# Optimization experiments

Measured on AMD Instinct MI355X. Metric: run time of the kernel, lower is better.

## Reference

```python
import jax, jax.numpy as jnp
import numpy as np

B, T, D, H = 2, 2048, 1024, 16
HD = D // H  # 64


def setup_inputs() -> dict:
    key = jax.random.key(0)
    ks = jax.random.split(key, 9)
    w = lambda k, shp: (jax.random.normal(k, shp, jnp.float32) * 0.02)
    return {
        "x": jax.random.normal(ks[0], (B, T, D), jnp.float32),
        "Wq": w(ks[1], (D, D)), "bq": jnp.zeros((D,), jnp.float32),
        "Wk": w(ks[2], (D, D)), "bk": jnp.zeros((D,), jnp.float32),
        "Wv": w(ks[3], (D, D)), "bv": jnp.zeros((D,), jnp.float32),
        "Wo": w(ks[4], (D, D)), "bo": jnp.zeros((D,), jnp.float32),
        "Wqs": w(ks[5], (3, HD)), "bqs": jnp.zeros((3,), jnp.float32),
        "Wks": w(ks[6], (3, HD)), "bks": jnp.zeros((3,), jnp.float32),
        "Wvs": w(ks[7], (3, HD)), "bvs": jnp.zeros((3,), jnp.float32),
        "temp": jnp.float32(1.0),
    }


def reference(x, Wq, bq, Wk, bk, Wv, bv, Wo, bo, Wqs, bqs, Wks, bks, Wvs, bvs, temp):
    Bx, Tx, Dx = x.shape
    # project and split heads: [B,H,T,HD]
    split = lambda y: y.reshape(Bx, Tx, H, HD).transpose(0, 2, 1, 3)
    q = split(x @ Wq.T + bq)
    k = split(x @ Wk.T + bk)
    v = split(x @ Wv.T + bv)
    # STP projections to 3-d: [B,H,T,3]
    q_stp = q @ Wqs.T + bqs
    k3 = k @ Wks.T + bks
    v3 = v @ Wvs.T + bvs
    # cross-product term (note: original's layernormed k_sub/v_sub are dead code)
    cross_kv = jnp.cross(k3, v3, axis=-1)  # [B,H,T,3]
    scores = (jnp.einsum('bhqd,bhkd->bhqk', q, k)
              + jnp.einsum('bhqc,bhkc->bhqk', q_stp, cross_kv)) * temp
    attn = jax.nn.softmax(scores, axis=-1)
    out = jnp.einsum('bhqk,bhkd->bhqd', attn, v)  # [B,H,T,HD]
    out = out.transpose(0, 2, 1, 3).reshape(Bx, Tx, Dx)
    return out @ Wo.T + bo
```

## Files before the change

### kernel.cpp

```cpp
#include <hip/hip_runtime.h>
#include <stdint.h>

typedef unsigned short u16;
typedef unsigned int u32;
typedef __attribute__((ext_vector_type(8))) short bf16x8;
typedef __attribute__((ext_vector_type(4))) float f32x4;
typedef __attribute__((ext_vector_type(4))) unsigned int u32x4;

__device__ __forceinline__ u16 f2b(float f) {
    union { float f; u32 u; } t; t.f = f;
    return (u16)((t.u + 0x7FFFu + ((t.u >> 16) & 1u)) >> 16);
}
__device__ __forceinline__ u32 pack2(float a, float b) {
    return (u32)f2b(a) | ((u32)f2b(b) << 16);
}
__device__ __forceinline__ u32 cvtpk2(float lo, float hi) {
    u32 r;
    asm("v_cvt_pk_bf16_f32 %0, %1, %2" : "=v"(r) : "v"(lo), "v"(hi));
    return r;
}
__device__ __forceinline__ void permlane32_swap(u32& a, u32& b) {
    asm("v_permlane32_swap_b32 %0, %1" : "+v"(a), "+v"(b));
}
__device__ __forceinline__ void permlane16_swap(u32& a, u32& b) {
    asm("v_permlane16_swap_b32 %0, %1" : "+v"(a), "+v"(b));
}

__device__ __forceinline__ void async_cp16(const u16* g, const u16* lds_base) {
    __builtin_amdgcn_global_load_lds(
        (const __attribute__((address_space(1))) void*)(uintptr_t)g,
        (__attribute__((address_space(3))) void*)(u32)(uintptr_t)lds_base,
        16, 0, 0);
}

__global__ void cast_all_kernel(const float* __restrict__ x,
                                const float* __restrict__ Wq, const float* __restrict__ Wk,
                                const float* __restrict__ Wv, const float* __restrict__ Wo,
                                u16* __restrict__ xb, u16* __restrict__ Wqb, u16* __restrict__ Wkb,
                                u16* __restrict__ Wvb, u16* __restrict__ Wob) {
    int i = blockIdx.x * blockDim.x + threadIdx.x;
    const float* s; u16* d; int off;
    if (i < 1048576) { s = x; d = xb; off = i; }
    else {
        int j = i - 1048576;
        int w = j >> 18; off = j & 262143;
        if (w == 0) { s = Wq; d = Wqb; }
        else if (w == 1) { s = Wk; d = Wkb; }
        else if (w == 2) { s = Wv; d = Wvb; }
        else { s = Wo; d = Wob; }
    }
    float4 f = ((const float4*)s)[off];
    ((uint2*)d)[off] = make_uint2(pack2(f.x, f.y), pack2(f.z, f.w));
}

__global__ __launch_bounds__(256) void gemm_qkv_kernel(
    const u16* __restrict__ xb,
    const u16* __restrict__ Wq, const u16* __restrict__ Wk, const u16* __restrict__ Wv,
    const float* __restrict__ bq, const float* __restrict__ bk, const float* __restrict__ bv,
    const float* __restrict__ Wqs, const float* __restrict__ bqs,
    const float* __restrict__ Wks, const float* __restrict__ bks,
    const float* __restrict__ Wvs, const float* __restrict__ bvs,
    const float* __restrict__ temp_p,
    u16* __restrict__ qe, u16* __restrict__ ke, u16* __restrict__ vT,
    float4* __restrict__ k3b, float4* __restrict__ v3b)
{
    __shared__ __align__(16) u16 As[2 * 64 * 32];
    __shared__ __align__(16) u16 Bs[2 * 128 * 32];
    const int tid = threadIdx.x;
    const int lane = tid & 63, w = tid >> 6;
    const int wm = w >> 1, wn = w & 1;
    const int l15 = lane & 15, quad = lane >> 4;
    const int M0 = blockIdx.y * 64, N0 = blockIdx.x * 128;
    const int bz = blockIdx.z;

    const u16* W = (bz == 0) ? Wq : (bz == 1) ? Wk : Wv;
    const float* bias = (bz == 0) ? bq : (bz == 1) ? bk : bv;
    const float* Wst = (bz == 0) ? Wqs : (bz == 1) ? Wks : Wvs;
    const float* bst = (bz == 0) ? bqs : (bz == 1) ? bks : bvs;

    f32x4 acc[2][4];
#pragma unroll
    for (int i = 0; i < 2; i++)
#pragma unroll
        for (int j = 0; j < 4; j++) acc[i][j] = (f32x4){0.f, 0.f, 0.f, 0.f};

    int ra = tid >> 2, ca = ((tid & 3) ^ (ra & 3)) * 8;
    const u16* Aga = xb + (size_t)(M0 + ra) * 1024 + ca;
    const u16* Bg0 = W + (size_t)(N0 + ra) * 1024 + ca;
    const u16* Bg1 = W + (size_t)(N0 + ra + 64) * 1024 + ca;
    const int aoff = (w * 64) * 8;
    const int boff0 = (w * 64) * 8;
    const int boff1 = (256 + w * 64) * 8;

    async_cp16(Aga, As + aoff);
    async_cp16(Bg0, Bs + boff0);
    async_cp16(Bg1, Bs + boff1);
    __syncthreads();

    for (int k0 = 0; k0 < 1024; k0 += 32) {
        const int buf = (k0 >> 5) & 1;
        const u16* Asr = As + buf * 2048;
        const u16* Bsr = Bs + buf * 4096;
        if (k0 + 32 < 1024) {
            const int nb_ = buf ^ 1;
            async_cp16(Aga + k0 + 32, As + nb_ * 2048 + aoff);
            async_cp16(Bg0 + k0 + 32, Bs + nb_ * 4096 + boff0);
            async_cp16(Bg1 + k0 + 32, Bs + nb_ * 4096 + boff1);
        }

        bf16x8 af[2], bf[4];
#pragma unroll
        for (int mi = 0; mi < 2; mi++)
            af[mi] = *(const bf16x8*)(Asr + (wm * 32 + mi * 16 + l15) * 32 + ((quad ^ (l15 & 3)) * 8));
#pragma unroll
        for (int ni = 0; ni < 4; ni++)
            bf[ni] = *(const bf16x8*)(Bsr + (wn * 64 + ni * 16 + l15) * 32 + ((quad ^ (l15 & 3)) * 8));
#pragma unroll
        for (int mi = 0; mi < 2; mi++)
#pragma unroll
            for (int ni = 0; ni < 4; ni++)
                acc[mi][ni] = __builtin_amdgcn_mfma_f32_16x16x32_bf16(af[mi], bf[ni], acc[mi][ni], 0, 0, 0);

        __syncthreads();
    }

    const float tau = temp_p[0] * 1.44269504088896f;
    const int nb = N0 + wn * 64;
    const int h = nb >> 6;
    float bias_v[4], wst_v[3][4];
#pragma unroll
    for (int ni = 0; ni < 4; ni++) {
        bias_v[ni] = bias[nb + ni * 16 + l15];
#pragma unroll
        for (int c = 0; c < 3; c++) wst_v[c][ni] = Wst[c * 64 + ni * 16 + l15];
    }
    const float bst0 = bst[0], bst1 = bst[1], bst2 = bst[2];

#pragma unroll
    for (int mi = 0; mi < 2; mi++) {
        int m0 = M0 + wm * 32 + mi * 16 + quad * 4;
        int b = m0 >> 11, t0 = m0 & 2047;
        float p0[4], p1[4], p2[4];
#pragma unroll
        for (int r = 0; r < 4; r++) {
            float a0 = 0.f, a1 = 0.f, a2 = 0.f;
#pragma unroll
            for (int ni = 0; ni < 4; ni++) {
                float v = acc[mi][ni][r] + bias_v[ni];
                a0 += v * wst_v[0][ni];
                a1 += v * wst_v[1][ni];
                a2 += v * wst_v[2][ni];
            }
#pragma unroll
            for (int off = 1; off < 16; off <<= 1) {
                a0 += __shfl_xor(a0, off);
                a1 += __shfl_xor(a1, off);
                a2 += __shfl_xor(a2, off);
            }
            p0[r] = a0 + bst0; p1[r] = a1 + bst1; p2[r] = a2 + bst2;
        }

        if (bz == 0) {
#pragma unroll
            for (int r = 0; r < 4; r++) {
                size_t row = (size_t)((b * 16 + h) * 2048 + (t0 + r));
                u16* qer = qe + row * 96;
#pragma unroll
                for (int ni = 0; ni < 4; ni++)
                    qer[ni * 16 + l15] = f2b((acc[mi][ni][r] + bias_v[ni]) * tau);
                if (l15 == 0) {
                    *(u32*)(qer + 64) = pack2(p0[r] * tau, p1[r] * tau);
                    *(u32*)(qer + 66) = (u32)f2b(p2[r] * tau);
                    uint2 z = make_uint2(0u, 0u);
#pragma unroll
                    for (int j = 68; j < 96; j += 4) *(uint2*)(qer + j) = z;
                }
            }
        } else if (bz == 1) {
#pragma unroll
            for (int r = 0; r < 4; r++) {
                size_t row = (size_t)((b * 16 + h) * 2048 + (t0 + r));
                u16* ker = ke + row * 96;
#pragma unroll
                for (int ni = 0; ni < 4; ni++)
                    ker[ni * 16 + l15] = f2b(acc[mi][ni][r] + bias_v[ni]);
                if (l15 == 0)
                    k3b[row] = make_float4(p0[r], p1[r], p2[r], 0.f);
            }
        } else {
#pragma unroll
            for (int ni = 0; ni < 4; ni++) {
                int hd = ni * 16 + l15;
                float v0 = acc[mi][ni][0] + bias_v[ni];
                float v1 = acc[mi][ni][1] + bias_v[ni];
                float v2 = acc[mi][ni][2] + bias_v[ni];
                float v3 = acc[mi][ni][3] + bias_v[ni];
                *(uint2*)(vT + ((size_t)((b * 16 + h) * 64 + hd)) * 2048 + t0) =
                    make_uint2(pack2(v0, v1), pack2(v2, v3));
            }
            if (l15 == 0) {
#pragma unroll
                for (int r = 0; r < 4; r++) {
                    size_t row = (size_t)((b * 16 + h) * 2048 + (t0 + r));
                    v3b[row] = make_float4(p0[r], p1[r], p2[r], 0.f);
                }
            }
        }
    }
}

__global__ void finish_ext_kernel(const float4* __restrict__ k3b, const float4* __restrict__ v3b,
                                  u16* __restrict__ ke)
{
    int row = blockIdx.x * blockDim.x + threadIdx.x;
    if (row >= 2 * 16 * 2048) return;
    float4 k3 = k3b[row];
    float4 v3 = v3b[row];
    float c0 = k3.y * v3.z - k3.z * v3.y;
    float c1 = k3.z * v3.x - k3.x * v3.z;
    float c2 = k3.x * v3.y - k3.y * v3.x;
    u16* ker = ke + (size_t)row * 96;
    *(u32*)(ker + 64) = pack2(c0, c1);
    *(u32*)(ker + 66) = (u32)f2b(c2);
    uint2 z = make_uint2(0u, 0u);
#pragma unroll
    for (int j = 68; j < 96; j += 4) *(uint2*)(ker + j) = z;
}

__global__ __launch_bounds__(256) void gemm_out_kernel(
    const u16* __restrict__ ao, const u16* __restrict__ Wo, const float* __restrict__ bo,
    float* __restrict__ out)
{
    __shared__ __align__(16) u16 As[2 * 64 * 32];
    __shared__ __align__(16) u16 Bs[2 * 128 * 32];
    const int tid = threadIdx.x;
    const int lane = tid & 63, w = tid >> 6;
    const int wm = w >> 1, wn = w & 1;
    const int l15 = lane & 15, quad = lane >> 4;
    const int M0 = blockIdx.y * 64, N0 = blockIdx.x * 128;

    f32x4 acc[2][4];
#pragma unroll
    for (int i = 0; i < 2; i++)
#pragma unroll
        for (int j = 0; j < 4; j++) acc[i][j] = (f32x4){0.f, 0.f, 0.f, 0.f};

    int ra = tid >> 2, ca = ((tid & 3) ^ (ra & 3)) * 8;
    const u16* Aga = ao + (size_t)(M0 + ra) * 1024 + ca;
    const u16* Bg0 = Wo + (size_t)(N0 + ra) * 1024 + ca;
    const u16* Bg1 = Wo + (size_t)(N0 + ra + 64) * 1024 + ca;
    const int aoff = (w * 64) * 8;
    const int boff0 = (w * 64) * 8;
    const int boff1 = (256 + w * 64) * 8;

    async_cp16(Aga, As + aoff);
    async_cp16(Bg0, Bs + boff0);
    async_cp16(Bg1, Bs + boff1);
    __syncthreads();

    for (int k0 = 0; k0 < 1024; k0 += 32) {
        const int buf = (k0 >> 5) & 1;
        const u16* Asr = As + buf * 2048;
        const u16* Bsr = Bs + buf * 4096;
        if (k0 + 32 < 1024) {
            const int nb_ = buf ^ 1;
            async_cp16(Aga + k0 + 32, As + nb_ * 2048 + aoff);
            async_cp16(Bg0 + k0 + 32, Bs + nb_ * 4096 + boff0);
            async_cp16(Bg1 + k0 + 32, Bs + nb_ * 4096 + boff1);
        }

        bf16x8 af[2], bf[4];
#pragma unroll
        for (int mi = 0; mi < 2; mi++)
            af[mi] = *(const bf16x8*)(Asr + (wm * 32 + mi * 16 + l15) * 32 + ((quad ^ (l15 & 3)) * 8));
#pragma unroll
        for (int ni = 0; ni < 4; ni++)
            bf[ni] = *(const bf16x8*)(Bsr + (wn * 64 + ni * 16 + l15) * 32 + ((quad ^ (l15 & 3)) * 8));
#pragma unroll
        for (int mi = 0; mi < 2; mi++)
#pragma unroll
            for (int ni = 0; ni < 4; ni++)
                acc[mi][ni] = __builtin_amdgcn_mfma_f32_16x16x32_bf16(af[mi], bf[ni], acc[mi][ni], 0, 0, 0);

        __syncthreads();
    }

#pragma unroll
    for (int mi = 0; mi < 2; mi++)
#pragma unroll
        for (int ni = 0; ni < 4; ni++) {
            int n = N0 + wn * 64 + ni * 16 + l15;
            float bias_n = bo[n];
            int m0 = M0 + wm * 32 + mi * 16 + quad * 4;
#pragma unroll
            for (int r = 0; r < 4; r++)
                out[(size_t)(m0 + r) * 1024 + n] = acc[mi][ni][r] + bias_n;
        }
}

__global__ __launch_bounds__(256, 2) void attn_kernel(
    const u16* __restrict__ qe, const u16* __restrict__ ke, const u16* __restrict__ vT,
    u16* __restrict__ out)
{
    __shared__ __align__(16) u16 smem[24576];
    u16* const KsA = smem;
    u16* const VtA = smem + 16384;

    const int tid = threadIdx.x;
    const int lane = tid & 63, w = tid >> 6;
    const int kw = w & 1, qw = w >> 1;
    const int l15 = lane & 15, quad = lane >> 4;
    const int lsw = l15 & 7;
    const int bh = blockIdx.y;
    const int q0 = blockIdx.x * 128;

    const u16* qeb = qe + (size_t)bh * 2048 * 96;
    const u16* keb = ke + (size_t)bh * 2048 * 96;
    const u16* vTb = vT + (size_t)bh * 64 * 2048;

    size_t koff[4];
#pragma unroll
    for (int j = 0; j < 4; j++) {
        int r = w * 16 + j * 4 + (lane >> 4);
        koff[j] = (size_t)r * 96 + (size_t)((((lane & 15) ^ (r & 7)) * 8));
    }
    size_t voff[2];
#pragma unroll
    for (int j = 0; j < 2; j++) {
        int r = w * 16 + j * 8 + (lane >> 3);
        voff[j] = (size_t)r * 2048 + (size_t)((((lane & 7) ^ (r & 7)) * 8));
    }

#pragma unroll
    for (int j = 0; j < 4; j++) async_cp16(keb + koff[j], KsA + w * 2048 + j * 512);
#pragma unroll
    for (int j = 0; j < 2; j++) async_cp16(vTb + voff[j], VtA + w * 1024 + j * 512);

    bf16x8 bq[4][3];
#pragma unroll
    for (int s = 0; s < 4; s++) {
        const u16* qrow = qeb + (size_t)(q0 + qw * 64 + s * 16 + l15) * 96;
#pragma unroll
        for (int ks = 0; ks < 3; ks++) bq[s][ks] = *(const bf16x8*)(qrow + ks * 32 + quad * 8);
    }

    f32x4 O[4][4];
    float l_part[4];
#pragma unroll
    for (int s = 0; s < 4; s++) {
        l_part[s] = 0.f;
#pragma unroll
        for (int dt = 0; dt < 4; dt++) O[s][dt] = (f32x4){0.f, 0.f, 0.f, 0.f};
    }

    __syncthreads();

    for (int kb = 0; kb < 2048; kb += 64) {
        const int buf = (kb >> 6) & 1;
        const u16* Ks = KsA + buf * 8192;
        const u16* Vt = VtA + buf * 4096;

        if (kb + 64 < 2048) {
            u16* Ksn = KsA + (buf ^ 1) * 8192;
            u16* Vtn = VtA + (buf ^ 1) * 4096;
            const size_t kb96 = (size_t)(kb + 64) * 96;
#pragma unroll
            for (int j = 0; j < 4; j++) async_cp16(keb + kb96 + koff[j], Ksn + w * 2048 + j * 512);
#pragma unroll
            for (int j = 0; j < 2; j++) async_cp16(vTb + (size_t)(kb + 64) + voff[j], Vtn + w * 1024 + j * 512);
        }

        f32x4 S[4][2];
#pragma unroll
        for (int s = 0; s < 4; s++)
#pragma unroll
            for (int nt = 0; nt < 2; nt++) S[s][nt] = (f32x4){0.f, 0.f, 0.f, 0.f};

        __builtin_amdgcn_s_setprio(1);
#pragma unroll
        for (int ks = 0; ks < 3; ks++) {
            bf16x8 ak[2];
#pragma unroll
            for (int nt = 0; nt < 2; nt++)
                ak[nt] = *(const bf16x8*)(Ks + (kw * 32 + nt * 16 + l15) * 128 + (((ks * 4 + quad) ^ lsw) & 15) * 8);
#pragma unroll
            for (int s = 0; s < 4; s++)
#pragma unroll
                for (int nt = 0; nt < 2; nt++)
                    S[s][nt] = __builtin_amdgcn_mfma_f32_16x16x32_bf16(ak[nt], bq[s][ks], S[s][nt], 0, 0, 0);
        }
        __builtin_amdgcn_s_setprio(0);

        bf16x8 av[4];
#pragma unroll
        for (int dt = 0; dt < 4; dt++)
            av[dt] = *(const bf16x8*)(Vt + (dt * 16 + l15) * 64 + (((kw * 4 + quad) ^ lsw) & 7) * 8);

#pragma unroll
        for (int s = 0; s < 4; s++) {
            float sum = 0.f;
#pragma unroll
            for (int nt = 0; nt < 2; nt++)
#pragma unroll
                for (int r = 0; r < 4; r++) {
                    float p = __builtin_amdgcn_exp2f(S[s][nt][r]);
                    S[s][nt][r] = p;
                    sum += p;
                }
            l_part[s] += sum;
            u32 a0 = cvtpk2(S[s][0][0], S[s][0][1]);
            u32 b0 = cvtpk2(S[s][1][0], S[s][1][1]);
            u32 a1 = cvtpk2(S[s][0][2], S[s][0][3]);
            u32 b1 = cvtpk2(S[s][1][2], S[s][1][3]);
            permlane32_swap(a0, b0);
            permlane32_swap(a1, b1);
            permlane16_swap(a0, b0);
            permlane16_swap(a1, b1);
            bf16x8 pv = __builtin_bit_cast(bf16x8, (u32x4){a0, a1, b0, b1});
            __builtin_amdgcn_s_setprio(1);
#pragma unroll
            for (int dt = 0; dt < 4; dt++)
                O[s][dt] = __builtin_amdgcn_mfma_f32_16x16x32_bf16(av[dt], pv, O[s][dt], 0, 0, 0);
            __builtin_amdgcn_s_setprio(0);
        }

        __syncthreads();
    }

    float* const Ored = (float*)smem;
    float* const Lr = (float*)(smem + 17664);
    if (kw == 1) {
#pragma unroll
        for (int s = 0; s < 4; s++) {
            float l = l_part[s];
            l += __shfl_xor(l, 16);
            l += __shfl_xor(l, 32);
            if (lane < 16) Lr[qw * 64 + s * 16 + l15] = l;
            int qrow = qw * 64 + s * 16 + l15;
#pragma unroll
            for (int dt = 0; dt < 4; dt++) {
                int dc = dt ^ (l15 & 3);
                *(float4*)(Ored + qrow * 68 + dc * 16 + quad * 4) =
                    make_float4(O[s][dt][0], O[s][dt][1], O[s][dt][2], O[s][dt][3]);
            }
        }
    }
    __syncthreads();
    if (kw == 0) {
        const int b = bh >> 4, h = bh & 15;
#pragma unroll
        for (int s = 0; s < 4; s++) {
            float l = l_part[s];
            l += __shfl_xor(l, 16);
            l += __shfl_xor(l, 32);
            int qrow = qw * 64 + s * 16 + l15;
            l += Lr[qrow];
            float linv = 1.0f / l;
            int tq = q0 + qrow;
#pragma unroll
            for (int dt = 0; dt < 4; dt++) {
                int dc = dt ^ (l15 & 3);
                float4 o2 = *(const float4*)(Ored + qrow * 68 + dc * 16 + quad * 4);
                int d = h * 64 + dt * 16 + quad * 4;
                *(uint2*)(out + (size_t)(b * 2048 + tq) * 1024 + d) =
                    make_uint2(cvtpk2((O[s][dt][0] + o2.x) * linv, (O[s][dt][1] + o2.y) * linv),
                               cvtpk2((O[s][dt][2] + o2.z) * linv, (O[s][dt][3] + o2.w) * linv));
            }
        }
    }
}

extern "C" void kernel_launch(void* const* d_in, const int* in_sizes, int n_in,
                              void* d_out, int out_size, void* d_ws, size_t ws_size,
                              hipStream_t stream)
{
    (void)in_sizes; (void)n_in; (void)out_size; (void)ws_size;
    const float* x   = (const float*)d_in[0];
    const float* Wq  = (const float*)d_in[1];
    const float* bq  = (const float*)d_in[2];
    const float* Wk  = (const float*)d_in[3];
    const float* bk  = (const float*)d_in[4];
    const float* Wv  = (const float*)d_in[5];
    const float* bv  = (const float*)d_in[6];
    const float* Wo  = (const float*)d_in[7];
    const float* bo  = (const float*)d_in[8];
    const float* Wqs = (const float*)d_in[9];
    const float* bqs = (const float*)d_in[10];
    const float* Wks = (const float*)d_in[11];
    const float* bks = (const float*)d_in[12];
    const float* Wvs = (const float*)d_in[13];
    const float* bvs = (const float*)d_in[14];
    const float* temp = (const float*)d_in[15];

    char* ws = (char*)d_ws;
    u16* xb  = (u16*)(ws);
    u16* Wqb = (u16*)(ws + 8388608);
    u16* Wkb = (u16*)(ws + 10485760);
    u16* Wvb = (u16*)(ws + 12582912);
    u16* Wob = (u16*)(ws + 14680064);
    u16* qeb = (u16*)(ws + 16777216);
    u16* keb = (u16*)(ws + 29360128);
    u16* vTb = (u16*)(ws + 41943040);
    float4* k3b = (float4*)(ws + 50331648);
    float4* v3b = (float4*)(ws + 51380224);
    u16* aob = (u16*)(ws + 52428800);

    cast_all_kernel<<<8192, 256, 0, stream>>>(x, Wq, Wk, Wv, Wo, xb, Wqb, Wkb, Wvb, Wob);
    gemm_qkv_kernel<<<dim3(8, 64, 3), 256, 0, stream>>>(
        xb, Wqb, Wkb, Wvb, bq, bk, bv, Wqs, bqs, Wks, bks, Wvs, bvs, temp,
        qeb, keb, vTb, k3b, v3b);
    finish_ext_kernel<<<256, 256, 0, stream>>>(k3b, v3b, keb);
    attn_kernel<<<dim3(16, 32), 256, 0, stream>>>(qeb, keb, vTb, aob);
    gemm_out_kernel<<<dim3(8, 64), 256, 0, stream>>>(aob, Wob, bo, (float*)d_out);
}
```

Before: 221.1 us.

## Fuse Q/K/V projections into one GEMM block sharing the x tile

The QKV projection kernel now has each block compute all three Q, K and V outputs for the same 64x128 tile. It loads the x tile once and reuses it across three weight tiles, instead of launching a z-dimension of 3 that reloads x each time. Accumulator count triples (96 floats per thread) and B-tile shared memory triples, which raises register pressure and lowers occupancy. Grid launches also change to a linear 1D index with M varying fastest, which alters block scheduling and L2 locality for both GEMMs.

```diff
diff --git a/kernel.cpp b/kernel.cpp
--- a/kernel.cpp
+++ b/kernel.cpp
@@ -65,61 +65,71 @@
     float4* __restrict__ k3b, float4* __restrict__ v3b)
 {
     __shared__ __align__(16) u16 As[2 * 64 * 32];
-    __shared__ __align__(16) u16 Bs[2 * 128 * 32];
+    __shared__ __align__(16) u16 Bs[3 * 2 * 128 * 32];
     const int tid = threadIdx.x;
     const int lane = tid & 63, w = tid >> 6;
     const int wm = w >> 1, wn = w & 1;
     const int l15 = lane & 15, quad = lane >> 4;
-    const int M0 = blockIdx.y * 64, N0 = blockIdx.x * 128;
-    const int bz = blockIdx.z;
-
-    const u16* W = (bz == 0) ? Wq : (bz == 1) ? Wk : Wv;
-    const float* bias = (bz == 0) ? bq : (bz == 1) ? bk : bv;
-    const float* Wst = (bz == 0) ? Wqs : (bz == 1) ? Wks : Wvs;
-    const float* bst = (bz == 0) ? bqs : (bz == 1) ? bks : bvs;
-
-    f32x4 acc[2][4];
-#pragma unroll
-    for (int i = 0; i < 2; i++)
-#pragma unroll
-        for (int j = 0; j < 4; j++) acc[i][j] = (f32x4){0.f, 0.f, 0.f, 0.f};
+    const int lin = blockIdx.x;
+    const int M0 = (lin & 63) * 64;
+    const int N0 = (lin >> 6) * 128;
+
+    f32x4 acc[3][2][4];
+#pragma unroll
+    for (int z = 0; z < 3; z++)
+#pragma unroll
+        for (int i = 0; i < 2; i++)
+#pragma unroll
+            for (int j = 0; j < 4; j++) acc[z][i][j] = (f32x4){0.f, 0.f, 0.f, 0.f};
 
     int ra = tid >> 2, ca = ((tid & 3) ^ (ra & 3)) * 8;
     const u16* Aga = xb + (size_t)(M0 + ra) * 1024 + ca;
-    const u16* Bg0 = W + (size_t)(N0 + ra) * 1024 + ca;
-    const u16* Bg1 = W + (size_t)(N0 + ra + 64) * 1024 + ca;
+    const u16* Bg0[3], *Bg1[3];
+    Bg0[0] = Wq + (size_t)(N0 + ra) * 1024 + ca;  Bg1[0] = Wq + (size_t)(N0 + ra + 64) * 1024 + ca;
+    Bg0[1] = Wk + (size_t)(N0 + ra) * 1024 + ca;  Bg1[1] = Wk + (size_t)(N0 + ra + 64) * 1024 + ca;
+    Bg0[2] = Wv + (size_t)(N0 + ra) * 1024 + ca;  Bg1[2] = Wv + (size_t)(N0 + ra + 64) * 1024 + ca;
     const int aoff = (w * 64) * 8;
     const int boff0 = (w * 64) * 8;
     const int boff1 = (256 + w * 64) * 8;
 
     async_cp16(Aga, As + aoff);
-    async_cp16(Bg0, Bs + boff0);
-    async_cp16(Bg1, Bs + boff1);
+#pragma unroll
+    for (int z = 0; z < 3; z++) {
+        async_cp16(Bg0[z], Bs + z * 8192 + boff0);
+        async_cp16(Bg1[z], Bs + z * 8192 + boff1);
+    }
     __syncthreads();
 
     for (int k0 = 0; k0 < 1024; k0 += 32) {
         const int buf = (k0 >> 5) & 1;
         const u16* Asr = As + buf * 2048;
-        const u16* Bsr = Bs + buf * 4096;
         if (k0 + 32 < 1024) {
             const int nb_ = buf ^ 1;
             async_cp16(Aga + k0 + 32, As + nb_ * 2048 + aoff);
-            async_cp16(Bg0 + k0 + 32, Bs + nb_ * 4096 + boff0);
-            async_cp16(Bg1 + k0 + 32, Bs + nb_ * 4096 + boff1);
-        }
-
-        bf16x8 af[2], bf[4];
+#pragma unroll
+            for (int z = 0; z < 3; z++) {
+                async_cp16(Bg0[z] + k0 + 32, Bs + z * 8192 + nb_ * 4096 + boff0);
+                async_cp16(Bg1[z] + k0 + 32, Bs + z * 8192 + nb_ * 4096 + boff1);
+            }
+        }
+
+        bf16x8 af[2];
 #pragma unroll
         for (int mi = 0; mi < 2; mi++)
             af[mi] = *(const bf16x8*)(Asr + (wm * 32 + mi * 16 + l15) * 32 + ((quad ^ (l15 & 3)) * 8));
 #pragma unroll
-        for (int ni = 0; ni < 4; ni++)
-            bf[ni] = *(const bf16x8*)(Bsr + (wn * 64 + ni * 16 + l15) * 32 + ((quad ^ (l15 & 3)) * 8));
-#pragma unroll
-        for (int mi = 0; mi < 2; mi++)
+        for (int z = 0; z < 3; z++) {
+            const u16* Bsr = Bs + z * 8192 + buf * 4096;
+            bf16x8 bf[4];
 #pragma unroll
             for (int ni = 0; ni < 4; ni++)
-                acc[mi][ni] = __builtin_amdgcn_mfma_f32_16x16x32_bf16(af[mi], bf[ni], acc[mi][ni], 0, 0, 0);
+                bf[ni] = *(const bf16x8*)(Bsr + (wn * 64 + ni * 16 + l15) * 32 + ((quad ^ (l15 & 3)) * 8));
+#pragma unroll
+            for (int mi = 0; mi < 2; mi++)
+#pragma unroll
+                for (int ni = 0; ni < 4; ni++)
+                    acc[z][mi][ni] = __builtin_amdgcn_mfma_f32_16x16x32_bf16(af[mi], bf[ni], acc[z][mi][ni], 0, 0, 0);
+        }
 
         __syncthreads();
     }
@@ -127,82 +137,89 @@
     const float tau = temp_p[0] * 1.44269504088896f;
     const int nb = N0 + wn * 64;
     const int h = nb >> 6;
-    float bias_v[4], wst_v[3][4];
-#pragma unroll
-    for (int ni = 0; ni < 4; ni++) {
-        bias_v[ni] = bias[nb + ni * 16 + l15];
-#pragma unroll
-        for (int c = 0; c < 3; c++) wst_v[c][ni] = Wst[c * 64 + ni * 16 + l15];
-    }
-    const float bst0 = bst[0], bst1 = bst[1], bst2 = bst[2];
-
-#pragma unroll
-    for (int mi = 0; mi < 2; mi++) {
-        int m0 = M0 + wm * 32 + mi * 16 + quad * 4;
-        int b = m0 >> 11, t0 = m0 & 2047;
-        float p0[4], p1[4], p2[4];
-#pragma unroll
-        for (int r = 0; r < 4; r++) {
-            float a0 = 0.f, a1 = 0.f, a2 = 0.f;
-#pragma unroll
-            for (int ni = 0; ni < 4; ni++) {
-                float v = acc[mi][ni][r] + bias_v[ni];
-                a0 += v * wst_v[0][ni];
-                a1 += v * wst_v[1][ni];
-                a2 += v * wst_v[2][ni];
+
+#pragma unroll
+    for (int z = 0; z < 3; z++) {
+        const float* bias = (z == 0) ? bq : (z == 1) ? bk : bv;
+        const float* Wst = (z == 0) ? Wqs : (z == 1) ? Wks : Wvs;
+        const float* bst = (z == 0) ? bqs : (z == 1) ? bks : bvs;
+        float bias_v[4], wst_v[3][4];
+#pragma unroll
+        for (int ni = 0; ni < 4; ni++) {
+            bias_v[ni] = bias[nb + ni * 16 + l15];
+#pragma unroll
+            for (int c = 0; c < 3; c++) wst_v[c][ni] = Wst[c * 64 + ni * 16 + l15];
+        }
+        const float bst0 = bst[0], bst1 = bst[1], bst2 = bst[2];
+
+#pragma unroll
+        for (int mi = 0; mi < 2; mi++) {
+            int m0 = M0 + wm * 32 + mi * 16 + quad * 4;
+            int b = m0 >> 11, t0 = m0 & 2047;
+            float p0[4], p1[4], p2[4];
+#pragma unroll
+            for (int r = 0; r < 4; r++) {
+                float a0 = 0.f, a1 = 0.f, a2 = 0.f;
+#pragma unroll
+                for (int ni = 0; ni < 4; ni++) {
+                    float v = acc[z][mi][ni][r] + bias_v[ni];
+                    a0 += v * wst_v[0][ni];
+                    a1 += v * wst_v[1][ni];
+                    a2 += v * wst_v[2][ni];
+                }
+#pragma unroll
+                for (int off = 1; off < 16; off <<= 1) {
+                    a0 += __shfl_xor(a0, off);
+                    a1 += __shfl_xor(a1, off);
+                    a2 += __shfl_xor(a2, off);
+                }
+                p0[r] = a0 + bst0; p1[r] = a1 + bst1; p2[r] = a2 + bst2;
             }
-#pragma unroll
-            for (int off = 1; off < 16; off <<= 1) {
-                a0 += __shfl_xor(a0, off);
-                a1 += __shfl_xor(a1, off);
-                a2 += __shfl_xor(a2, off);
-            }
-            p0[r] = a0 + bst0; p1[r] = a1 + bst1; p2[r] = a2 + bst2;
-        }
-
-        if (bz == 0) {
-#pragma unroll
-            for (int r = 0; r < 4; r++) {
-                size_t row = (size_t)((b * 16 + h) * 2048 + (t0 + r));
-                u16* qer = qe + row * 96;
-#pragma unroll
-                for (int ni = 0; ni < 4; ni++)
-                    qer[ni * 16 + l15] = f2b((acc[mi][ni][r] + bias_v[ni]) * tau);
-                if (l15 == 0) {
-                    *(u32*)(qer + 64) = pack2(p0[r] * tau, p1[r] * tau);
-                    *(u32*)(qer + 66) = (u32)f2b(p2[r] * tau);
-                    uint2 z = make_uint2(0u, 0u);
-#pragma unroll
-                    for (int j = 68; j < 96; j += 4) *(uint2*)(qer + j) = z;
-                }
-            }
-        } else if (bz == 1) {
-#pragma unroll
-            for (int r = 0; r < 4; r++) {
-                size_t row = (size_t)((b * 16 + h) * 2048 + (t0 + r));
-                u16* ker = ke + row * 96;
-#pragma unroll
-                for (int ni = 0; ni < 4; ni++)
-                    ker[ni * 16 + l15] = f2b(acc[mi][ni][r] + bias_v[ni]);
-                if (l15 == 0)
-                    k3b[row] = make_float4(p0[r], p1[r], p2[r], 0.f);
-            }
-        } else {
-#pragma unroll
-            for (int ni = 0; ni < 4; ni++) {
-                int hd = ni * 16 + l15;
-                float v0 = acc[mi][ni][0] + bias_v[ni];
-                float v1 = acc[mi][ni][1] + bias_v[ni];
-                float v2 = acc[mi][ni][2] + bias_v[ni];
-                float v3 = acc[mi][ni][3] + bias_v[ni];
-                *(uint2*)(vT + ((size_t)((b * 16 + h) * 64 + hd)) * 2048 + t0) =
-                    make_uint2(pack2(v0, v1), pack2(v2, v3));
-            }
-            if (l15 == 0) {
+
+            if (z == 0) {
 #pragma unroll
                 for (int r = 0; r < 4; r++) {
                     size_t row = (size_t)((b * 16 + h) * 2048 + (t0 + r));
-                    v3b[row] = make_float4(p0[r], p1[r], p2[r], 0.f);
+                    u16* qer = qe + row * 96;
+#pragma unroll
+                    for (int ni = 0; ni < 4; ni++)
+                        qer[ni * 16 + l15] = f2b((acc[z][mi][ni][r] + bias_v[ni]) * tau);
+                    if (l15 == 0) {
+                        *(u32*)(qer + 64) = pack2(p0[r] * tau, p1[r] * tau);
+                        *(u32*)(qer + 66) = (u32)f2b(p2[r] * tau);
+                        uint2 zz = make_uint2(0u, 0u);
+#pragma unroll
+                        for (int j = 68; j < 96; j += 4) *(uint2*)(qer + j) = zz;
+                    }
+                }
+            } else if (z == 1) {
+#pragma unroll
+                for (int r = 0; r < 4; r++) {
+                    size_t row = (size_t)((b * 16 + h) * 2048 + (t0 + r));
+                    u16* ker = ke + row * 96;
+#pragma unroll
+                    for (int ni = 0; ni < 4; ni++)
+                        ker[ni * 16 + l15] = f2b(acc[z][mi][ni][r] + bias_v[ni]);
+                    if (l15 == 0)
+                        k3b[row] = make_float4(p0[r], p1[r], p2[r], 0.f);
+                }
+            } else {
+#pragma unroll
+                for (int ni = 0; ni < 4; ni++) {
+                    int hd = ni * 16 + l15;
+                    float v0 = acc[z][mi][ni][0] + bias_v[ni];
+                    float v1 = acc[z][mi][ni][1] + bias_v[ni];
+                    float v2 = acc[z][mi][ni][2] + bias_v[ni];
+                    float v3 = acc[z][mi][ni][3] + bias_v[ni];
+                    *(uint2*)(vT + ((size_t)((b * 16 + h) * 64 + hd)) * 2048 + t0) =
+                        make_uint2(pack2(v0, v1), pack2(v2, v3));
+                }
+                if (l15 == 0) {
+#pragma unroll
+                    for (int r = 0; r < 4; r++) {
+                        size_t row = (size_t)((b * 16 + h) * 2048 + (t0 + r));
+                        v3b[row] = make_float4(p0[r], p1[r], p2[r], 0.f);
+                    }
                 }
             }
         }
@@ -237,7 +254,9 @@
     const int lane = tid & 63, w = tid >> 6;
     const int wm = w >> 1, wn = w & 1;
     const int l15 = lane & 15, quad = lane >> 4;
-    const int M0 = blockIdx.y * 64, N0 = blockIdx.x * 128;
+    const int lin = blockIdx.x;
+    const int M0 = (lin & 63) * 64;
+    const int N0 = (lin >> 6) * 128;
 
     f32x4 acc[2][4];
 #pragma unroll
@@ -506,10 +525,10 @@
     u16* aob = (u16*)(ws + 52428800);
 
     cast_all_kernel<<<8192, 256, 0, stream>>>(x, Wq, Wk, Wv, Wo, xb, Wqb, Wkb, Wvb, Wob);
-    gemm_qkv_kernel<<<dim3(8, 64, 3), 256, 0, stream>>>(
+    gemm_qkv_kernel<<<512, 256, 0, stream>>>(
         xb, Wqb, Wkb, Wvb, bq, bk, bv, Wqs, bqs, Wks, bks, Wvs, bvs, temp,
         qeb, keb, vTb, k3b, v3b);
     finish_ext_kernel<<<256, 256, 0, stream>>>(k3b, v3b, keb);
     attn_kernel<<<dim3(16, 32), 256, 0, stream>>>(qeb, keb, vTb, aob);
-    gemm_out_kernel<<<dim3(8, 64), 256, 0, stream>>>(aob, Wob, bo, (float*)d_out);
-}
+    gemm_out_kernel<<<512, 256, 0, stream>>>(aob, Wob, bo, (float*)d_out);
+}
```

Measured after the change: 231.4 us. +4.7%, slower.
